# Kernel tuning notes

Hardware: AMD Instinct MI355X
Metric: run time of the kernel (lower is better)

The kernel has to match this reference:

```python
import jax, jax.numpy as jnp
import numpy as np

N, E, D, K = 32768, 16384, 4, 8          # nodes, hyperedges, edges/node, nodes/edge
IN_DIM, OUT_DIM, EDGE_DIM, NUM_HEADS = 128, 128, 64, 8


def setup_inputs() -> dict:
    key = jax.random.key(0)
    ks = jax.random.split(key, 16)
    s_in = 1.0 / np.sqrt(IN_DIM)
    s_out = 1.0 / np.sqrt(OUT_DIM)
    s_edge = 1.0 / np.sqrt(EDGE_DIM)
    return {
        "x": jax.random.normal(ks[0], (N, IN_DIM), jnp.float32),
        "edge_attr": jax.random.normal(ks[1], (E, EDGE_DIM), jnp.float32),
        "node_edges": jax.random.randint(ks[2], (N, D), 0, E),   # hyperedges containing each node
        "edge_nodes": jax.random.randint(ks[3], (E, K), 0, N),   # nodes inside each hyperedge
        "W_lin": jax.random.normal(ks[4], (OUT_DIM, IN_DIM), jnp.float32) * s_in,
        "W_edge": jax.random.normal(ks[5], (OUT_DIM, EDGE_DIM), jnp.float32) * s_edge,
        "Wq": jax.random.normal(ks[6], (OUT_DIM, OUT_DIM), jnp.float32) * s_out,
        "Wk": jax.random.normal(ks[7], (OUT_DIM, OUT_DIM), jnp.float32) * s_out,
        "Wv": jax.random.normal(ks[8], (OUT_DIM, OUT_DIM), jnp.float32) * s_out,
        "bq": jnp.zeros((OUT_DIM,), jnp.float32),
        "bk": jnp.zeros((OUT_DIM,), jnp.float32),
        "bv": jnp.zeros((OUT_DIM,), jnp.float32),
        "Wo": jax.random.normal(ks[9], (OUT_DIM, OUT_DIM), jnp.float32) * s_out,
        "bo": jnp.zeros((OUT_DIM,), jnp.float32),
    }


def reference(x, edge_attr, node_edges, edge_nodes,
              W_lin, W_edge, Wq, Wk, Wv, bq, bk, bv, Wo, bo):
    n, out_dim = x.shape[0], W_lin.shape[0]
    hd = out_dim // NUM_HEADS
    L = node_edges.shape[1] * edge_nodes.shape[1]  # D*K keys per node

    Wh = x @ W_lin.T                               # [N, out]
    We = edge_attr @ W_edge.T                      # [E, out]

    u_idx = edge_nodes[node_edges]                 # [N, D, K] neighbor node ids
    vals = Wh[u_idx]                               # [N, D, K, out]
    keys = vals + We[node_edges][:, :, None, :]    # key = Wh[u] + We[e]
    keys = keys.reshape(n, L, out_dim)
    vals = vals.reshape(n, L, out_dim)

    # torch nn.MultiheadAttention: single query per node (query = Wh[v])
    q = (Wh @ Wq.T + bq).reshape(n, NUM_HEADS, hd)
    k = (keys @ Wk.T + bk).reshape(n, L, NUM_HEADS, hd)
    v = (vals @ Wv.T + bv).reshape(n, L, NUM_HEADS, hd)

    scores = jnp.einsum('nhd,nlhd->nhl', q, k) / jnp.sqrt(jnp.asarray(hd, q.dtype))
    attn = jax.nn.softmax(scores, axis=-1)         # [N, H, L]
    ctx = jnp.einsum('nhl,nlhd->nhd', attn, v).reshape(n, out_dim)
    out = ctx @ Wo.T + bo
    return jax.nn.relu(out)
```

## Files before the change

kernel.cpp:

```cpp
#include <hip/hip_runtime.h>
#include <hip/hip_cooperative_groups.h>

namespace cg = cooperative_groups;

#define N_NODES 32768
#define N_EDGES 16384
#define DEG 4
#define KPE 8
#define DIM 128
#define EDIM 64

#define GRID_BLOCKS 512
#define ATTN_WAVES (GRID_BLOCKS * 4)

#define AOFF_K 0
#define AOFF_E 8704
#define AOFF_P 9792
#define AWAVESZ 10944

typedef float f32x4 __attribute__((ext_vector_type(4)));
typedef __bf16 bf16x8 __attribute__((ext_vector_type(8)));
typedef __bf16 bf16x2 __attribute__((ext_vector_type(2)));
typedef unsigned short u16x8 __attribute__((ext_vector_type(8)));
typedef unsigned int u32;
typedef unsigned int u32x4 __attribute__((ext_vector_type(4)));

static __device__ __forceinline__ unsigned short f2bf(float f) {
  union { float f; unsigned int u; } v; v.f = f;
  unsigned int r = (v.u + 0x7FFFu + ((v.u >> 16) & 1u)) >> 16;
  return (unsigned short)r;
}
static __device__ __forceinline__ float bflo(unsigned int v) {
  union { unsigned int u; float f; } x; x.u = v << 16; return x.f;
}
static __device__ __forceinline__ float bfhi(unsigned int v) {
  union { unsigned int u; float f; } x; x.u = v & 0xffff0000u; return x.f;
}

#if __has_builtin(__builtin_amdgcn_fdot2_f32_bf16)
static __device__ __forceinline__ float dot2bf(unsigned int a, unsigned int b, float c) {
  return __builtin_amdgcn_fdot2_f32_bf16(
      __builtin_bit_cast(bf16x2, a), __builtin_bit_cast(bf16x2, b), c, false);
}
#else
static __device__ __forceinline__ float dot2bf(unsigned int a, unsigned int b, float c) {
  c = fmaf(bflo(a), bflo(b), c);
  return fmaf(bfhi(a), bfhi(b), c);
}
#endif

#define GLDS(gp, ldsp, sz) __builtin_amdgcn_global_load_lds(               \
    (const __attribute__((address_space(1))) u32*)(gp),                    \
    (__attribute__((address_space(3))) u32*)(ldsp), sz, 0, 0)


static __device__ __forceinline__ void wprep_elem(
    int id, const float* __restrict__ Wq, const float* __restrict__ Wk,
    const float* __restrict__ Wv, const float* __restrict__ Wlin,
    const float* __restrict__ Wedge, const float* __restrict__ Wo,
    unsigned short* __restrict__ CW, unsigned short* __restrict__ CWE,
    unsigned short* __restrict__ Wob)
{
  if (id < 384 * 128) {
    int j = id >> 7, i = id & 127;
    const float* wrow; float scale = 1.0f;
    if (j < 128)      { wrow = Wq + j * 128; scale = 0.25f; }
    else if (j < 256) { wrow = Wk + (j - 128) * 128; }
    else              { wrow = Wv + (j - 256) * 128; }
    float s = 0.f;
    #pragma unroll 8
    for (int m = 0; m < 128; ++m) s += wrow[m] * Wlin[m * 128 + i];
    CW[id] = f2bf(s * scale);
  } else if (id < 384 * 128 + 128 * 64) {
    int id2 = id - 384 * 128; int j = id2 >> 6, t = id2 & 63;
    float s = 0.f;
    #pragma unroll 8
    for (int m = 0; m < 128; ++m) s += Wk[j * 128 + m] * Wedge[m * 64 + t];
    CWE[id2] = f2bf(s);
  } else if (id < 384 * 128 + 128 * 64 + 128 * 128) {
    int id3 = id - (384 * 128 + 128 * 64);
    Wob[id3] = f2bf(Wo[id3]);
  }
}

static __device__ __forceinline__ void g12_unit(
    int unit, int wave, int lane,
    const float* __restrict__ x, const unsigned short* __restrict__ CW,
    const float* __restrict__ bq, const float* __restrict__ bv,
    unsigned short* __restrict__ qb, unsigned short* __restrict__ Kb,
    unsigned short* __restrict__ Vb,
    const float* __restrict__ ea, const unsigned short* __restrict__ CWE,
    const float* __restrict__ bk, unsigned short* __restrict__ WeKb)
{
  const int r16 = lane & 15, quad = lane >> 4;
  if (unit < 512) {
    const int m0 = unit * 64 + wave * 16;
    u16x8 av[4];
    const float* arow = x + (size_t)(m0 + r16) * DIM + quad * 8;
    #pragma unroll
    for (int kk = 0; kk < 4; ++kk) {
      float4 a0 = *(const float4*)(arow + kk * 32);
      float4 a1 = *(const float4*)(arow + kk * 32 + 4);
      u16x8 au;
      au[0] = f2bf(a0.x); au[1] = f2bf(a0.y); au[2] = f2bf(a0.z); au[3] = f2bf(a0.w);
      au[4] = f2bf(a1.x); au[5] = f2bf(a1.y); au[6] = f2bf(a1.z); au[7] = f2bf(a1.w);
      av[kk] = au;
    }
    #pragma unroll
    for (int g = 0; g < 6; ++g) {
      f32x4 acc[4];
      const f32x4 z = {0.f, 0.f, 0.f, 0.f};
      acc[0] = z; acc[1] = z; acc[2] = z; acc[3] = z;
      #pragma unroll
      for (int kk = 0; kk < 4; ++kk) {
        #pragma unroll
        for (int s = 0; s < 4; ++s) {
          u16x8 bu = *(const u16x8*)(CW + (size_t)(g * 64 + s * 16 + r16) * DIM + kk * 32 + quad * 8);
          acc[s] = __builtin_amdgcn_mfma_f32_16x16x32_bf16(
              __builtin_bit_cast(bf16x8, av[kk]), __builtin_bit_cast(bf16x8, bu), acc[s], 0, 0, 0);
        }
      }
      const int arr = g >> 1;
      const int colbase = (g & 1) * 64;
      unsigned short* dst = arr == 0 ? qb : (arr == 1 ? Kb : Vb);
      #pragma unroll
      for (int s = 0; s < 4; ++s) {
        int j = colbase + s * 16 + r16;
        float bias = arr == 0 ? 0.25f * bq[j] : (arr == 2 ? bv[j] : 0.f);
        #pragma unroll
        for (int r = 0; r < 4; ++r) {
          int m = m0 + quad * 4 + r;
          dst[(size_t)m * DIM + j] = f2bf(acc[s][r] + bias);
        }
      }
    }
  } else {
    const int idx = unit - 512;
    const int m0 = (idx >> 1) * 64 + wave * 16;
    const int n0 = (idx & 1) * 64;
    f32x4 acc[4];
    const f32x4 z = {0.f, 0.f, 0.f, 0.f};
    acc[0] = z; acc[1] = z; acc[2] = z; acc[3] = z;
    const float* arow = ea + (size_t)(m0 + r16) * EDIM + quad * 8;
    #pragma unroll
    for (int kk = 0; kk < 2; ++kk) {
      float4 a0 = *(const float4*)(arow + kk * 32);
      float4 a1 = *(const float4*)(arow + kk * 32 + 4);
      u16x8 au;
      au[0] = f2bf(a0.x); au[1] = f2bf(a0.y); au[2] = f2bf(a0.z); au[3] = f2bf(a0.w);
      au[4] = f2bf(a1.x); au[5] = f2bf(a1.y); au[6] = f2bf(a1.z); au[7] = f2bf(a1.w);
      bf16x8 av = __builtin_bit_cast(bf16x8, au);
      #pragma unroll
      for (int s = 0; s < 4; ++s) {
        u16x8 bu = *(const u16x8*)(CWE + (size_t)(n0 + s * 16 + r16) * EDIM + kk * 32 + quad * 8);
        acc[s] = __builtin_amdgcn_mfma_f32_16x16x32_bf16(
            av, __builtin_bit_cast(bf16x8, bu), acc[s], 0, 0, 0);
      }
    }
    #pragma unroll
    for (int s = 0; s < 4; ++s) {
      int j = n0 + s * 16 + r16;
      float bias = bk[j];
      #pragma unroll
      for (int r = 0; r < 4; ++r) {
        int m = m0 + quad * 4 + r;
        WeKb[(size_t)m * DIM + j] = f2bf(acc[s][r] + bias);
      }
    }
  }
}

static __device__ __forceinline__ void attn_node(
    int n, unsigned char* __restrict__ abuf, int lane,
    const unsigned short* __restrict__ qb, const unsigned short* __restrict__ Kb,
    const unsigned short* __restrict__ Vb, const unsigned short* __restrict__ WeKb,
    const int* __restrict__ nedges, const int* __restrict__ enodes,
    unsigned short* __restrict__ ctxb)
{
  float* ldsP = (float*)(abuf + AOFF_P);
  const int l = lane & 31, half = lane >> 5;
  const int h = lane >> 3;
  const int c0 = lane * 2;

  int4 e4 = *(const int4*)(nedges + (size_t)n * DEG);
  int4 m0i = *(const int4*)(enodes + (size_t)e4.x * KPE);
  int4 m1i = *(const int4*)(enodes + (size_t)e4.x * KPE + 4);
  int4 m2i = *(const int4*)(enodes + (size_t)e4.y * KPE);
  int4 m3i = *(const int4*)(enodes + (size_t)e4.y * KPE + 4);
  int4 m4i = *(const int4*)(enodes + (size_t)e4.z * KPE);
  int4 m5i = *(const int4*)(enodes + (size_t)e4.z * KPE + 4);
  int4 m6i = *(const int4*)(enodes + (size_t)e4.w * KPE);
  int4 m7i = *(const int4*)(enodes + (size_t)e4.w * KPE + 4);

#define STAGE(off, table, row) GLDS((const u32*)((table) + (size_t)(row) * DIM) + lane, abuf + (off), 4)
  STAGE(AOFF_K + 0  * 272, Kb, m0i.x); STAGE(AOFF_K + 1  * 272, Kb, m0i.y);
  STAGE(AOFF_K + 2  * 272, Kb, m0i.z); STAGE(AOFF_K + 3  * 272, Kb, m0i.w);
  STAGE(AOFF_K + 4  * 272, Kb, m1i.x); STAGE(AOFF_K + 5  * 272, Kb, m1i.y);
  STAGE(AOFF_K + 6  * 272, Kb, m1i.z); STAGE(AOFF_K + 7  * 272, Kb, m1i.w);
  STAGE(AOFF_K + 8  * 272, Kb, m2i.x); STAGE(AOFF_K + 9  * 272, Kb, m2i.y);
  STAGE(AOFF_K + 10 * 272, Kb, m2i.z); STAGE(AOFF_K + 11 * 272, Kb, m2i.w);
  STAGE(AOFF_K + 12 * 272, Kb, m3i.x); STAGE(AOFF_K + 13 * 272, Kb, m3i.y);
  STAGE(AOFF_K + 14 * 272, Kb, m3i.z); STAGE(AOFF_K + 15 * 272, Kb, m3i.w);
  STAGE(AOFF_K + 16 * 272, Kb, m4i.x); STAGE(AOFF_K + 17 * 272, Kb, m4i.y);
  STAGE(AOFF_K + 18 * 272, Kb, m4i.z); STAGE(AOFF_K + 19 * 272, Kb, m4i.w);
  STAGE(AOFF_K + 20 * 272, Kb, m5i.x); STAGE(AOFF_K + 21 * 272, Kb, m5i.y);
  STAGE(AOFF_K + 22 * 272, Kb, m5i.z); STAGE(AOFF_K + 23 * 272, Kb, m5i.w);
  STAGE(AOFF_K + 24 * 272, Kb, m6i.x); STAGE(AOFF_K + 25 * 272, Kb, m6i.y);
  STAGE(AOFF_K + 26 * 272, Kb, m6i.z); STAGE(AOFF_K + 27 * 272, Kb, m6i.w);
  STAGE(AOFF_K + 28 * 272, Kb, m7i.x); STAGE(AOFF_K + 29 * 272, Kb, m7i.y);
  STAGE(AOFF_K + 30 * 272, Kb, m7i.z); STAGE(AOFF_K + 31 * 272, Kb, m7i.w);
  STAGE(AOFF_E + 0 * 272, WeKb, e4.x); STAGE(AOFF_E + 1 * 272, WeKb, e4.y);
  STAGE(AOFF_E + 2 * 272, WeKb, e4.z); STAGE(AOFF_E + 3 * 272, WeKb, e4.w);
#undef STAGE

  const u32x4* qp = (const u32x4*)(qb + (size_t)n * DIM + half * 64);
  u32x4 qv[8];
  #pragma unroll
  for (int ch = 0; ch < 8; ++ch) qv[ch] = __builtin_nontemporal_load(qp + ch);

  asm volatile("" ::: "memory");

  u32 vv[32];
#define VLOAD(t, row) vv[t] = *(const u32*)(Vb + (size_t)(row) * DIM + c0)
  VLOAD(0,  m0i.x); VLOAD(1,  m0i.y); VLOAD(2,  m0i.z); VLOAD(3,  m0i.w);
  VLOAD(4,  m1i.x); VLOAD(5,  m1i.y); VLOAD(6,  m1i.z); VLOAD(7,  m1i.w);
  VLOAD(8,  m2i.x); VLOAD(9,  m2i.y); VLOAD(10, m2i.z); VLOAD(11, m2i.w);
  VLOAD(12, m3i.x); VLOAD(13, m3i.y); VLOAD(14, m3i.z); VLOAD(15, m3i.w);
  VLOAD(16, m4i.x); VLOAD(17, m4i.y); VLOAD(18, m4i.z); VLOAD(19, m4i.w);
  VLOAD(20, m5i.x); VLOAD(21, m5i.y); VLOAD(22, m5i.z); VLOAD(23, m5i.w);
  VLOAD(24, m6i.x); VLOAD(25, m6i.y); VLOAD(26, m6i.z); VLOAD(27, m6i.w);
  VLOAD(28, m7i.x); VLOAD(29, m7i.y); VLOAD(30, m7i.z); VLOAD(31, m7i.w);
#undef VLOAD

  asm volatile("s_waitcnt vmcnt(32)" ::: "memory");

  const unsigned char* krow = abuf + AOFF_K + l * 272 + half * 128;
  const unsigned char* erow = abuf + AOFF_E + (l >> 3) * 272 + half * 128;
  float s[4] = {0.f, 0.f, 0.f, 0.f};
  #pragma unroll
  for (int ch = 0; ch < 8; ++ch) {
    uint4 kc = *(const uint4*)(krow + ch * 16);
    uint4 ec = *(const uint4*)(erow + ch * 16);
    const int hi = ch >> 1;
    float t = s[hi];
    t = dot2bf(qv[ch].x, kc.x, t); t = dot2bf(qv[ch].x, ec.x, t);
    t = dot2bf(qv[ch].y, kc.y, t); t = dot2bf(qv[ch].y, ec.y, t);
    t = dot2bf(qv[ch].z, kc.z, t); t = dot2bf(qv[ch].z, ec.z, t);
    t = dot2bf(qv[ch].w, kc.w, t); t = dot2bf(qv[ch].w, ec.w, t);
    s[hi] = t;
  }

  #pragma unroll
  for (int hi = 0; hi < 4; ++hi) {
    float vmax = s[hi];
    #pragma unroll
    for (int off = 16; off >= 1; off >>= 1)
      vmax = fmaxf(vmax, __shfl_xor(vmax, off, 32));
    float ex = __expf(s[hi] - vmax);
    float sum = ex;
    #pragma unroll
    for (int off = 16; off >= 1; off >>= 1)
      sum += __shfl_xor(sum, off, 32);
    ldsP[(half * 4 + hi) * 36 + l] = ex / sum;
  }

  float a0 = 0.f, a1 = 0.f;
  #pragma unroll
  for (int t = 0; t < 8; ++t) {
    float4 p4 = *(const float4*)(ldsP + h * 36 + t * 4);
    a0 = fmaf(p4.x, bflo(vv[t * 4 + 0]), a0); a1 = fmaf(p4.x, bfhi(vv[t * 4 + 0]), a1);
    a0 = fmaf(p4.y, bflo(vv[t * 4 + 1]), a0); a1 = fmaf(p4.y, bfhi(vv[t * 4 + 1]), a1);
    a0 = fmaf(p4.z, bflo(vv[t * 4 + 2]), a0); a1 = fmaf(p4.z, bfhi(vv[t * 4 + 2]), a1);
    a0 = fmaf(p4.w, bflo(vv[t * 4 + 3]), a0); a1 = fmaf(p4.w, bfhi(vv[t * 4 + 3]), a1);
  }
  unsigned int pk = (unsigned int)f2bf(a0) | ((unsigned int)f2bf(a1) << 16);
  __builtin_nontemporal_store(pk, (u32*)(ctxb + (size_t)n * DIM + c0));
}

static __device__ __forceinline__ void g4_unit(
    int unit, int wave, int lane,
    const unsigned short* __restrict__ ctxb, const unsigned short* __restrict__ Wob,
    const float* __restrict__ bo, float* __restrict__ out)
{
  const int r16 = lane & 15, quad = lane >> 4;
  const int bx = unit & 511, by = unit >> 9;
  const int m0 = bx * 64 + wave * 16;
  const int n0 = by * 64;
  f32x4 acc[4];
  const f32x4 z = {0.f, 0.f, 0.f, 0.f};
  acc[0] = z; acc[1] = z; acc[2] = z; acc[3] = z;
  #pragma unroll
  for (int kk = 0; kk < 4; ++kk) {
    u16x8 au = *(const u16x8*)(ctxb + (size_t)(m0 + r16) * DIM + kk * 32 + quad * 8);
    bf16x8 av = __builtin_bit_cast(bf16x8, au);
    #pragma unroll
    for (int s = 0; s < 4; ++s) {
      u16x8 bu = *(const u16x8*)(Wob + (size_t)(n0 + s * 16 + r16) * DIM + kk * 32 + quad * 8);
      acc[s] = __builtin_amdgcn_mfma_f32_16x16x32_bf16(
          av, __builtin_bit_cast(bf16x8, bu), acc[s], 0, 0, 0);
    }
  }
  #pragma unroll
  for (int s = 0; s < 4; ++s) {
    int j = n0 + s * 16 + r16;
    float bias = bo[j];
    #pragma unroll
    for (int r = 0; r < 4; ++r) {
      int m = m0 + quad * 4 + r;
      float v = acc[s][r] + bias;
      out[(size_t)m * DIM + j] = v > 0.f ? v : 0.f;
    }
  }
}

__global__ __launch_bounds__(256, 2) void fused_kernel(
    const float* __restrict__ x, const float* __restrict__ ea,
    const int* __restrict__ nedges, const int* __restrict__ enodes,
    const float* __restrict__ Wlin, const float* __restrict__ Wedge,
    const float* __restrict__ Wq, const float* __restrict__ Wk,
    const float* __restrict__ Wv, const float* __restrict__ bq,
    const float* __restrict__ bk, const float* __restrict__ bv,
    const float* __restrict__ Wo, const float* __restrict__ bo,
    unsigned short* __restrict__ CW, unsigned short* __restrict__ CWE,
    unsigned short* __restrict__ Wob, unsigned short* __restrict__ qb,
    unsigned short* __restrict__ Kb, unsigned short* __restrict__ Vb,
    unsigned short* __restrict__ WeKb, unsigned short* __restrict__ ctxb,
    float* __restrict__ out)
{
  __shared__ __align__(16) unsigned char slds[AWAVESZ * 4];
  cg::grid_group grid = cg::this_grid();
  const int wave = threadIdx.x >> 6, lane = threadIdx.x & 63;

  wprep_elem(blockIdx.x * 256 + threadIdx.x, Wq, Wk, Wv, Wlin, Wedge, Wo, CW, CWE, Wob);
  grid.sync();

  for (int unit = blockIdx.x; unit < 1024; unit += GRID_BLOCKS)
    g12_unit(unit, wave, lane, x, CW, bq, bv, qb, Kb, Vb, ea, CWE, bk, WeKb);
  grid.sync();

  {
    unsigned char* abuf = slds + wave * AWAVESZ;
    const int wv = blockIdx.x * 4 + wave;
    for (int n = wv; n < N_NODES; n += ATTN_WAVES)
      attn_node(n, abuf, lane, qb, Kb, Vb, WeKb, nedges, enodes, ctxb);
  }
  grid.sync();

  for (int unit = blockIdx.x; unit < 1024; unit += GRID_BLOCKS)
    g4_unit(unit, wave, lane, ctxb, Wob, bo, out);
}

__global__ __launch_bounds__(256) void wprep_kernel(
    const float* __restrict__ Wq, const float* __restrict__ Wk,
    const float* __restrict__ Wv, const float* __restrict__ Wlin,
    const float* __restrict__ Wedge, const float* __restrict__ Wo,
    unsigned short* __restrict__ CW, unsigned short* __restrict__ CWE,
    unsigned short* __restrict__ Wob)
{
  wprep_elem(blockIdx.x * 256 + threadIdx.x, Wq, Wk, Wv, Wlin, Wedge, Wo, CW, CWE, Wob);
}

__global__ __launch_bounds__(256) void g12_kernel(
    const float* __restrict__ x, const unsigned short* __restrict__ CW,
    const float* __restrict__ bq, const float* __restrict__ bv,
    unsigned short* __restrict__ qb, unsigned short* __restrict__ Kb,
    unsigned short* __restrict__ Vb,
    const float* __restrict__ ea, const unsigned short* __restrict__ CWE,
    const float* __restrict__ bk, unsigned short* __restrict__ WeKb)
{
  g12_unit(blockIdx.x, threadIdx.x >> 6, threadIdx.x & 63,
           x, CW, bq, bv, qb, Kb, Vb, ea, CWE, bk, WeKb);
}

__global__ __launch_bounds__(256, 2) void attn_kernel(
    const unsigned short* __restrict__ qb, const unsigned short* __restrict__ Kb,
    const unsigned short* __restrict__ Vb, const unsigned short* __restrict__ WeKb,
    const int* __restrict__ nedges, const int* __restrict__ enodes,
    unsigned short* __restrict__ ctxb)
{
  __shared__ __align__(16) unsigned char slds[AWAVESZ * 4];
  const int wave = threadIdx.x >> 6, lane = threadIdx.x & 63;
  attn_node(blockIdx.x * 4 + wave, slds + wave * AWAVESZ, lane,
            qb, Kb, Vb, WeKb, nedges, enodes, ctxb);
}

__global__ __launch_bounds__(256) void g4_kernel(
    const unsigned short* __restrict__ ctxb, const unsigned short* __restrict__ Wob,
    const float* __restrict__ bo, float* __restrict__ out)
{
  g4_unit(blockIdx.x, threadIdx.x >> 6, threadIdx.x & 63, ctxb, Wob, bo, out);
}

extern "C" void kernel_launch(void* const* d_in, const int* in_sizes, int n_in,
                              void* d_out, int out_size, void* d_ws, size_t ws_size,
                              hipStream_t stream)
{
  const float* x     = (const float*)d_in[0];
  const float* ea    = (const float*)d_in[1];
  const int* nedges  = (const int*)d_in[2];
  const int* enodes  = (const int*)d_in[3];
  const float* Wlin  = (const float*)d_in[4];
  const float* Wedge = (const float*)d_in[5];
  const float* Wq    = (const float*)d_in[6];
  const float* Wk    = (const float*)d_in[7];
  const float* Wv    = (const float*)d_in[8];
  const float* bq    = (const float*)d_in[9];
  const float* bk    = (const float*)d_in[10];
  const float* bv    = (const float*)d_in[11];
  const float* Wo    = (const float*)d_in[12];
  const float* bo    = (const float*)d_in[13];
  float* out = (float*)d_out;

  unsigned short* wsp = (unsigned short*)d_ws;
  unsigned short* CW   = wsp;  wsp += 384 * 128;
  unsigned short* CWE  = wsp;  wsp += 128 * 64;
  unsigned short* Wob  = wsp;  wsp += 128 * 128;
  unsigned short* qb   = wsp;  wsp += (size_t)N_NODES * DIM;
  unsigned short* Kb   = wsp;  wsp += (size_t)N_NODES * DIM;
  unsigned short* Vb   = wsp;  wsp += (size_t)N_NODES * DIM;
  unsigned short* WeKb = wsp;  wsp += (size_t)N_EDGES * DIM;
  unsigned short* ctxb = wsp;  wsp += (size_t)N_NODES * DIM;

  int maxb = 0;
  hipError_t qerr = hipOccupancyMaxActiveBlocksPerMultiprocessor(
      &maxb, (const void*)fused_kernel, 256, 0);
  bool coop = (qerr == hipSuccess && maxb >= 2);

  if (coop) {
    void* args[] = {
      (void*)&x, (void*)&ea, (void*)&nedges, (void*)&enodes,
      (void*)&Wlin, (void*)&Wedge, (void*)&Wq, (void*)&Wk, (void*)&Wv,
      (void*)&bq, (void*)&bk, (void*)&bv, (void*)&Wo, (void*)&bo,
      (void*)&CW, (void*)&CWE, (void*)&Wob, (void*)&qb, (void*)&Kb,
      (void*)&Vb, (void*)&WeKb, (void*)&ctxb, (void*)&out
    };
    hipError_t le = hipLaunchCooperativeKernel((const void*)fused_kernel,
                                               dim3(GRID_BLOCKS), dim3(256),
                                               args, 0, stream);
    if (le == hipSuccess) return;
  }

  wprep_kernel<<<dim3(288), dim3(256), 0, stream>>>(Wq, Wk, Wv, Wlin, Wedge, Wo, CW, CWE, Wob);
  g12_kernel<<<dim3(1024), dim3(256), 0, stream>>>(x, CW, bq, bv, qb, Kb, Vb, ea, CWE, bk, WeKb);
  attn_kernel<<<dim3(8192), dim3(256), 0, stream>>>(qb, Kb, Vb, WeKb, nedges, enodes, ctxb);
  g4_kernel<<<dim3(1024), dim3(256), 0, stream>>>(ctxb, Wob, bo, out);
}
```

Measured before the change: 207.7 us.

## Replace cooperative persistent kernel with four separate kernel launches

Removes the cooperative fused kernel with grid-wide syncs and always runs the four-kernel path (weight prep, projections, attention, output GEMM). This drops three grid barriers and the fixed 512-block persistent grid, letting each stage use its natural grid size. The attention kernel's launch bounds are raised to 3 blocks per CU to allow more occupancy. In exchange it pays extra kernel launch gaps, and the higher occupancy target may force register spills.

```diff
diff --git a/kernel.cpp b/kernel.cpp
--- a/kernel.cpp
+++ b/kernel.cpp
@@ -1,7 +1,4 @@
 #include <hip/hip_runtime.h>
-#include <hip/hip_cooperative_groups.h>
-
-namespace cg = cooperative_groups;
 
 #define N_NODES 32768
 #define N_EDGES 16384
@@ -10,9 +7,6 @@
 #define DIM 128
 #define EDIM 64
 
-#define GRID_BLOCKS 512
-#define ATTN_WAVES (GRID_BLOCKS * 4)
-
 #define AOFF_K 0
 #define AOFF_E 8704
 #define AOFF_P 9792
@@ -53,14 +47,14 @@
     (const __attribute__((address_space(1))) u32*)(gp),                    \
     (__attribute__((address_space(3))) u32*)(ldsp), sz, 0, 0)
 
-
-static __device__ __forceinline__ void wprep_elem(
-    int id, const float* __restrict__ Wq, const float* __restrict__ Wk,
+__global__ __launch_bounds__(256) void wprep_kernel(
+    const float* __restrict__ Wq, const float* __restrict__ Wk,
     const float* __restrict__ Wv, const float* __restrict__ Wlin,
     const float* __restrict__ Wedge, const float* __restrict__ Wo,
     unsigned short* __restrict__ CW, unsigned short* __restrict__ CWE,
     unsigned short* __restrict__ Wob)
 {
+  int id = blockIdx.x * 256 + threadIdx.x;
   if (id < 384 * 128) {
     int j = id >> 7, i = id & 127;
     const float* wrow; float scale = 1.0f;
@@ -83,8 +77,7 @@
   }
 }
 
-static __device__ __forceinline__ void g12_unit(
-    int unit, int wave, int lane,
+__global__ __launch_bounds__(256) void g12_kernel(
     const float* __restrict__ x, const unsigned short* __restrict__ CW,
     const float* __restrict__ bq, const float* __restrict__ bv,
     unsigned short* __restrict__ qb, unsigned short* __restrict__ Kb,
@@ -92,7 +85,10 @@
     const float* __restrict__ ea, const unsigned short* __restrict__ CWE,
     const float* __restrict__ bk, unsigned short* __restrict__ WeKb)
 {
+  const int wave = threadIdx.x >> 6, lane = threadIdx.x & 63;
   const int r16 = lane & 15, quad = lane >> 4;
+  const int unit = blockIdx.x;
+
   if (unit < 512) {
     const int m0 = unit * 64 + wave * 16;
     u16x8 av[4];
@@ -277,13 +273,25 @@
   __builtin_nontemporal_store(pk, (u32*)(ctxb + (size_t)n * DIM + c0));
 }
 
-static __device__ __forceinline__ void g4_unit(
-    int unit, int wave, int lane,
+__global__ __launch_bounds__(256, 3) void attn_kernel(
+    const unsigned short* __restrict__ qb, const unsigned short* __restrict__ Kb,
+    const unsigned short* __restrict__ Vb, const unsigned short* __restrict__ WeKb,
+    const int* __restrict__ nedges, const int* __restrict__ enodes,
+    unsigned short* __restrict__ ctxb)
+{
+  __shared__ __align__(16) unsigned char slds[AWAVESZ * 4];
+  const int wave = threadIdx.x >> 6, lane = threadIdx.x & 63;
+  attn_node(blockIdx.x * 4 + wave, slds + wave * AWAVESZ, lane,
+            qb, Kb, Vb, WeKb, nedges, enodes, ctxb);
+}
+
+__global__ __launch_bounds__(256) void g4_kernel(
     const unsigned short* __restrict__ ctxb, const unsigned short* __restrict__ Wob,
     const float* __restrict__ bo, float* __restrict__ out)
 {
+  const int wave = threadIdx.x >> 6, lane = threadIdx.x & 63;
   const int r16 = lane & 15, quad = lane >> 4;
-  const int bx = unit & 511, by = unit >> 9;
+  const int bx = blockIdx.x & 511, by = blockIdx.x >> 9;
   const int m0 = bx * 64 + wave * 16;
   const int n0 = by * 64;
   f32x4 acc[4];
@@ -311,84 +319,6 @@
       out[(size_t)m * DIM + j] = v > 0.f ? v : 0.f;
     }
   }
-}
-
-__global__ __launch_bounds__(256, 2) void fused_kernel(
-    const float* __restrict__ x, const float* __restrict__ ea,
-    const int* __restrict__ nedges, const int* __restrict__ enodes,
-    const float* __restrict__ Wlin, const float* __restrict__ Wedge,
-    const float* __restrict__ Wq, const float* __restrict__ Wk,
-    const float* __restrict__ Wv, const float* __restrict__ bq,
-    const float* __restrict__ bk, const float* __restrict__ bv,
-    const float* __restrict__ Wo, const float* __restrict__ bo,
-    unsigned short* __restrict__ CW, unsigned short* __restrict__ CWE,
-    unsigned short* __restrict__ Wob, unsigned short* __restrict__ qb,
-    unsigned short* __restrict__ Kb, unsigned short* __restrict__ Vb,
-    unsigned short* __restrict__ WeKb, unsigned short* __restrict__ ctxb,
-    float* __restrict__ out)
-{
-  __shared__ __align__(16) unsigned char slds[AWAVESZ * 4];
-  cg::grid_group grid = cg::this_grid();
-  const int wave = threadIdx.x >> 6, lane = threadIdx.x & 63;
-
-  wprep_elem(blockIdx.x * 256 + threadIdx.x, Wq, Wk, Wv, Wlin, Wedge, Wo, CW, CWE, Wob);
-  grid.sync();
-
-  for (int unit = blockIdx.x; unit < 1024; unit += GRID_BLOCKS)
-    g12_unit(unit, wave, lane, x, CW, bq, bv, qb, Kb, Vb, ea, CWE, bk, WeKb);
-  grid.sync();
-
-  {
-    unsigned char* abuf = slds + wave * AWAVESZ;
-    const int wv = blockIdx.x * 4 + wave;
-    for (int n = wv; n < N_NODES; n += ATTN_WAVES)
-      attn_node(n, abuf, lane, qb, Kb, Vb, WeKb, nedges, enodes, ctxb);
-  }
-  grid.sync();
-
-  for (int unit = blockIdx.x; unit < 1024; unit += GRID_BLOCKS)
-    g4_unit(unit, wave, lane, ctxb, Wob, bo, out);
-}
-
-__global__ __launch_bounds__(256) void wprep_kernel(
-    const float* __restrict__ Wq, const float* __restrict__ Wk,
-    const float* __restrict__ Wv, const float* __restrict__ Wlin,
-    const float* __restrict__ Wedge, const float* __restrict__ Wo,
-    unsigned short* __restrict__ CW, unsigned short* __restrict__ CWE,
-    unsigned short* __restrict__ Wob)
-{
-  wprep_elem(blockIdx.x * 256 + threadIdx.x, Wq, Wk, Wv, Wlin, Wedge, Wo, CW, CWE, Wob);
-}
-
-__global__ __launch_bounds__(256) void g12_kernel(
-    const float* __restrict__ x, const unsigned short* __restrict__ CW,
-    const float* __restrict__ bq, const float* __restrict__ bv,
-    unsigned short* __restrict__ qb, unsigned short* __restrict__ Kb,
-    unsigned short* __restrict__ Vb,
-    const float* __restrict__ ea, const unsigned short* __restrict__ CWE,
-    const float* __restrict__ bk, unsigned short* __restrict__ WeKb)
-{
-  g12_unit(blockIdx.x, threadIdx.x >> 6, threadIdx.x & 63,
-           x, CW, bq, bv, qb, Kb, Vb, ea, CWE, bk, WeKb);
-}
-
-__global__ __launch_bounds__(256, 2) void attn_kernel(
-    const unsigned short* __restrict__ qb, const unsigned short* __restrict__ Kb,
-    const unsigned short* __restrict__ Vb, const unsigned short* __restrict__ WeKb,
-    const int* __restrict__ nedges, const int* __restrict__ enodes,
-    unsigned short* __restrict__ ctxb)
-{
-  __shared__ __align__(16) unsigned char slds[AWAVESZ * 4];
-  const int wave = threadIdx.x >> 6, lane = threadIdx.x & 63;
-  attn_node(blockIdx.x * 4 + wave, slds + wave * AWAVESZ, lane,
-            qb, Kb, Vb, WeKb, nedges, enodes, ctxb);
-}
-
-__global__ __launch_bounds__(256) void g4_kernel(
-    const unsigned short* __restrict__ ctxb, const unsigned short* __restrict__ Wob,
-    const float* __restrict__ bo, float* __restrict__ out)
-{
-  g4_unit(blockIdx.x, threadIdx.x >> 6, threadIdx.x & 63, ctxb, Wob, bo, out);
 }
 
 extern "C" void kernel_launch(void* const* d_in, const int* in_sizes, int n_in,
@@ -421,25 +351,6 @@
   unsigned short* WeKb = wsp;  wsp += (size_t)N_EDGES * DIM;
   unsigned short* ctxb = wsp;  wsp += (size_t)N_NODES * DIM;
 
-  int maxb = 0;
-  hipError_t qerr = hipOccupancyMaxActiveBlocksPerMultiprocessor(
-      &maxb, (const void*)fused_kernel, 256, 0);
-  bool coop = (qerr == hipSuccess && maxb >= 2);
-
-  if (coop) {
-    void* args[] = {
-      (void*)&x, (void*)&ea, (void*)&nedges, (void*)&enodes,
-      (void*)&Wlin, (void*)&Wedge, (void*)&Wq, (void*)&Wk, (void*)&Wv,
-      (void*)&bq, (void*)&bk, (void*)&bv, (void*)&Wo, (void*)&bo,
-      (void*)&CW, (void*)&CWE, (void*)&Wob, (void*)&qb, (void*)&Kb,
-      (void*)&Vb, (void*)&WeKb, (void*)&ctxb, (void*)&out
-    };
-    hipError_t le = hipLaunchCooperativeKernel((const void*)fused_kernel,
-                                               dim3(GRID_BLOCKS), dim3(256),
-                                               args, 0, stream);
-    if (le == hipSuccess) return;
-  }
-
   wprep_kernel<<<dim3(288), dim3(256), 0, stream>>>(Wq, Wk, Wv, Wlin, Wedge, Wo, CW, CWE, Wob);
   g12_kernel<<<dim3(1024), dim3(256), 0, stream>>>(x, CW, bq, bv, qb, Kb, Vb, ea, CWE, bk, WeKb);
   attn_kernel<<<dim3(8192), dim3(256), 0, stream>>>(qb, Kb, Vb, WeKb, nedges, enodes, ctxb);
```

Result: no change. 205.7 us (-1.0%).
